# Kernel optimization log

Measured on AMD Instinct MI355X. Metric: run time of the kernel, lower is better.

## Reference

```python
import jax, jax.numpy as jnp
import numpy as np

B, C, H, W = 32, 512, 32, 32


def setup_inputs() -> dict:
    key = jax.random.key(0)
    ks = jax.random.split(key, 7)
    c2 = C // 2
    s_in = (1.0 / C) ** 0.5   # torch Conv2d default init scale (kernel 1x1)
    s_c2 = (1.0 / c2) ** 0.5
    return {
        "x": jax.random.normal(ks[0], (B, C, H, W), jnp.float32),
        "Wk": jax.random.normal(ks[1], (c2, C), jnp.float32) * s_in,
        "bk": jax.random.normal(ks[2], (c2,), jnp.float32) * s_in,
        "Wv": jax.random.normal(ks[3], (c2, C), jnp.float32) * s_in,
        "bv": jax.random.normal(ks[4], (c2,), jnp.float32) * s_in,
        "Wo": jax.random.normal(ks[5], (C, c2), jnp.float32) * s_c2,
        "bo": jax.random.normal(ks[6], (C,), jnp.float32) * s_c2,
    }


def reference(x, Wk, bk, Wv, bv, Wo, bo):
    Bn, Cn, Hn, Wn = x.shape
    c2 = Cn // 2
    M = Hn * Wn
    # 1x1 convs as channel contractions
    k = jnp.einsum('oc,bchw->bohw', Wk, x) + bk[None, :, None, None]   # [B,c2,H,W]
    v = jnp.einsum('oc,bchw->bohw', Wv, x) + bv[None, :, None, None]   # [B,c2,H,W]
    # torch .reshape(B, M, c2) reinterprets memory (NOT a transpose) -> same in jnp
    v = v.reshape(Bn, M, c2)                                           # [B,M,c2]
    kf = k.reshape(Bn, c2, M)                                          # [B,c2,M]
    # cov_feature: k^T I_hat k with I_hat = (1/M)I - (1/M^2)11^T
    #            = (1/M) k^T k - (1/M^2) s s^T,  s = sum over channels
    gram = jnp.einsum('bcm,bcn->bmn', kf, kf) / M                      # [B,M,M]
    s = kf.sum(axis=1)                                                 # [B,M]
    cov = gram - (s[:, :, None] * s[:, None, :]) / (M * M)
    attn = jax.nn.softmax(cov * (c2 ** -0.5), axis=-1)                 # [B,M,M]
    out = jnp.einsum('bmn,bnc->bmc', attn, v)                          # [B,M,c2]
    # torch .view(B, c2, H, W) is also a raw memory reinterpretation
    out = out.reshape(Bn, c2, Hn, Wn)
    out = jnp.einsum('oc,bchw->bohw', Wo, out) + bo[None, :, None, None]
    return out + x
```

## Files before the change

kernel.cpp:

```cpp
#include <hip/hip_runtime.h>


typedef short bf8 __attribute__((ext_vector_type(8)));
typedef float f32x4 __attribute__((ext_vector_type(4)));

#define MFMA16(a, b, c) __builtin_amdgcn_mfma_f32_16x16x32_bf16((a), (b), (c), 0, 0, 0)

__device__ __forceinline__ short f2bf(float x) {
  unsigned u = __float_as_uint(x);
  u += 0x7fffu + ((u >> 16) & 1u);
  return (short)(u >> 16);
}

__device__ __forceinline__ void gll16(const short* g, void* l) {
  __builtin_amdgcn_global_load_lds(
      (const __attribute__((address_space(1))) unsigned int*)g,
      (__attribute__((address_space(3))) unsigned int*)l, 16, 0, 0);
}

__device__ __forceinline__ void lgkm0() {
  asm volatile("s_waitcnt lgkmcnt(0)" ::: "memory");
}
template <int N>
__device__ __forceinline__ void waitv() {
  static_assert(N == 0 || N == 4 || N == 8, "bad vmcnt");
  if constexpr (N == 0) asm volatile("s_waitcnt vmcnt(0)" ::: "memory");
  else if constexpr (N == 4) asm volatile("s_waitcnt vmcnt(4)" ::: "memory");
  else asm volatile("s_waitcnt vmcnt(8)" ::: "memory");
}
__device__ __forceinline__ void barrier_relaxed() {
  asm volatile("" ::: "memory");
  __builtin_amdgcn_s_barrier();
  asm volatile("" ::: "memory");
}

__device__ __forceinline__ void gemm_core(const short* __restrict__ A,
                                          const short* __restrict__ B,
                                          int ldA, int ldB, int ksteps,
                                          char* smem, f32x4 acc[4][4]) {
  const int tid = threadIdx.x;
  const int w = tid >> 6, l = tid & 63;
  const int q = l >> 4, i = l & 15;
  const int wm = w & 1, wn = w >> 1;
  const int srow = l >> 3;
  const int gcol = ((l & 7) ^ srow) * 8;
  f32x4 zz = {0.f, 0.f, 0.f, 0.f};
  #pragma unroll
  for (int mt = 0; mt < 4; ++mt)
    #pragma unroll
    for (int nt = 0; nt < 4; ++nt) acc[mt][nt] = zz;

  for (int ks = 0; ks < ksteps; ++ks) {
    __syncthreads();
    const short* Ak = A + ks * 64 + gcol;
    const short* Bk = B + ks * 64 + gcol;
    #pragma unroll
    for (int j = 0; j < 4; ++j) {
      int s = w * 4 + j;
      size_t row = (size_t)(s * 8 + srow);
      gll16(Ak + row * ldA, smem + s * 1024);
      gll16(Bk + row * ldB, smem + 16384 + s * 1024);
    }
    __syncthreads();
    #pragma unroll
    for (int kq = 0; kq < 2; ++kq) {
      int sw = ((kq * 4 + q) ^ (i & 7)) * 16;
      bf8 af[4], bq[4];
      #pragma unroll
      for (int mt = 0; mt < 4; ++mt)
        af[mt] = *(const bf8*)(smem + (wm * 64 + mt * 16 + i) * 128 + sw);
      #pragma unroll
      for (int nt = 0; nt < 4; ++nt)
        bq[nt] = *(const bf8*)(smem + 16384 + (wn * 64 + nt * 16 + i) * 128 + sw);
      #pragma unroll
      for (int mt = 0; mt < 4; ++mt)
        #pragma unroll
        for (int nt = 0; nt < 4; ++nt)
          acc[mt][nt] = MFMA16(af[mt], bq[nt], acc[mt][nt]);
    }
  }
}

__global__ __launch_bounds__(256) void p0_xpose(const float* __restrict__ x,
                                                short* __restrict__ xT) {
  __shared__ float lds[64][65];
  int cb = blockIdx.x, sb = blockIdx.y, b = blockIdx.z;
  int t = threadIdx.x;
  int c0 = cb * 64, sp0 = sb * 64;
  const float4* x4 = reinterpret_cast<const float4*>(x);
  #pragma unroll
  for (int j = 0; j < 4; ++j) {
    int lin = t + 256 * j;
    int cl = lin >> 4, s4 = lin & 15;
    float4 v = x4[(((size_t)b * 512 + c0 + cl) * 1024 + sp0 + s4 * 4) >> 2];
    lds[cl][s4 * 4 + 0] = v.x; lds[cl][s4 * 4 + 1] = v.y;
    lds[cl][s4 * 4 + 2] = v.z; lds[cl][s4 * 4 + 3] = v.w;
  }
  __syncthreads();
  int spl = t >> 2, cs = (t & 3) * 16;
  bf8 o0, o1;
  #pragma unroll
  for (int j = 0; j < 8; ++j) o0[j] = f2bf(lds[cs + j][spl]);
  #pragma unroll
  for (int j = 0; j < 8; ++j) o1[j] = f2bf(lds[cs + 8 + j][spl]);
  size_t base = ((size_t)b * 1024 + sp0 + spl) * 512 + c0 + cs;
  *reinterpret_cast<bf8*>(xT + base) = o0;
  *reinterpret_cast<bf8*>(xT + base + 8) = o1;
}

__global__ __launch_bounds__(256) void w0_weights(const float* __restrict__ Wk,
                                                  const float* __restrict__ Wv,
                                                  const float* __restrict__ Wo,
                                                  short* __restrict__ Wkv_bf,
                                                  short* __restrict__ Wo_bf) {
  int g = blockIdx.x * 256 + threadIdx.x;
  if (g < 262144) {
    int o = g >> 9, c = g & 511;
    float v = (o < 256) ? Wk[o * 512 + c] : Wv[(o - 256) * 512 + c];
    Wkv_bf[g] = f2bf(v);
  } else {
    int i2 = g - 262144;
    Wo_bf[i2] = f2bf(Wo[i2]);
  }
}

__global__ __launch_bounds__(256, 2) void k1_kv(const short* __restrict__ xT,
                                                const short* __restrict__ Wkv,
                                                const float* __restrict__ bk,
                                                const float* __restrict__ bv,
                                                short* __restrict__ kT,
                                                short* __restrict__ vT,
                                                float* __restrict__ s_part) {
  __shared__ __attribute__((aligned(16))) char smem[36864];
  f32x4 acc[4][4];
  int bm = blockIdx.x, bn = blockIdx.y;
  gemm_core(xT + (size_t)bm * 128 * 512, Wkv + (size_t)bn * 128 * 512,
            512, 512, 8, smem, acc);
  int tid = threadIdx.x;
  int w = tid >> 6, l = tid & 63, q = l >> 4, i = l & 15;
  int wm = w & 1, wn = w >> 1;
  int mbase = bm * 128 + wm * 64;
  int nbase = bn * 128 + wn * 64;
  if (bn < 2) {
    __syncthreads();
    short* st = (short*)smem + w * 4352;
    float rp[4][4];
    #pragma unroll
    for (int mt = 0; mt < 4; ++mt)
      #pragma unroll
      for (int r = 0; r < 4; ++r) rp[mt][r] = 0.f;
    #pragma unroll
    for (int mt = 0; mt < 4; ++mt)
      #pragma unroll
      for (int nt = 0; nt < 4; ++nt) {
        float bias = bk[nbase + nt * 16 + i];
        #pragma unroll
        for (int r = 0; r < 4; ++r) {
          float val = acc[mt][nt][r] + bias;
          st[(mt * 16 + q * 4 + r) * 68 + nt * 16 + i] = f2bf(val);
          rp[mt][r] += val;
        }
      }
    lgkm0();
    #pragma unroll
    for (int j = 0; j < 8; ++j) {
      int row = j * 8 + (l >> 3), cc = l & 7;
      bf8 vv = *(const bf8*)(st + row * 68 + cc * 8);
      *(bf8*)(kT + (size_t)(mbase + row) * 256 + nbase + cc * 8) = vv;
    }
    #pragma unroll
    for (int mask = 1; mask <= 8; mask <<= 1)
      #pragma unroll
      for (int mt = 0; mt < 4; ++mt)
        #pragma unroll
        for (int r = 0; r < 4; ++r) rp[mt][r] += __shfl_xor(rp[mt][r], mask, 64);
    if (i == 0) {
      int pg = bn * 2 + wn;
      #pragma unroll
      for (int mt = 0; mt < 4; ++mt)
        #pragma unroll
        for (int r = 0; r < 4; ++r)
          s_part[pg * 32768 + mbase + mt * 16 + q * 4 + r] = rp[mt][r];
    }
  } else {
    #pragma unroll
    for (int mt = 0; mt < 4; ++mt)
      #pragma unroll
      for (int nt = 0; nt < 4; ++nt) {
        int o2 = nbase + nt * 16 + i - 256;
        float bias = bv[o2];
        #pragma unroll
        for (int r = 0; r < 4; ++r) {
          float val = acc[mt][nt][r] + bias;
          int mg = mbase + mt * 16 + q * 4 + r;
          int b = mg >> 10, sp = mg & 1023;
          vT[((size_t)b * 256 + (sp & 255)) * 1024 + 4 * o2 + (sp >> 8)] = f2bf(val);
        }
      }
  }
}

__global__ __launch_bounds__(256, 2) void k2_fused(const short* __restrict__ kT,
                                                   const short* __restrict__ vT,
                                                   const float* __restrict__ s_part,
                                                   short* __restrict__ OB) {
  __shared__ __attribute__((aligned(16))) char smem[81920];
  char* Apan = smem;
  char* Ppan = smem + 32768;
  char* Bst  = smem + 49152;

  const int id = blockIdx.x;
  const int xcd = id & 7, slot = id >> 3;
  const int b  = xcd * 4 + (slot >> 4);
  const int bm = slot & 15;

  const int tid = threadIdx.x;
  const int w = tid >> 6, l = tid & 63;
  const int q = l >> 4, i = l & 15;
  const int srow = l >> 3;
  const int gcol = ((l & 7) ^ srow) * 8;

  const short* kTb = kT + (size_t)b * 1024 * 256;
  const short* vTb = vT + (size_t)b * 256 * 1024;

  char* slabA = Bst + w * 4096;
  char* slabB = Bst + 16384 + w * 4096;

  const float sc1 = 1.0f / 16384.0f;
  const float sc2 = 1.0f / 16777216.0f;

  {
    const short* Am = kTb + (size_t)bm * 64 * 256;
    #pragma unroll
    for (int ks = 0; ks < 4; ++ks)
      #pragma unroll
      for (int j2 = 0; j2 < 2; ++j2) {
        int s2 = w * 2 + j2;
        gll16(Am + (size_t)(s2 * 8 + srow) * 256 + ks * 64 + gcol,
              Apan + ks * 8192 + s2 * 1024);
      }
  }

  const int mglob = b * 1024;
  float sm2[4][4];
  #pragma unroll
  for (int mt = 0; mt < 4; ++mt)
    #pragma unroll
    for (int r = 0; r < 4; ++r) {
      int m = mglob + bm * 64 + mt * 16 + q * 4 + r;
      sm2[mt][r] = (s_part[m] + s_part[32768 + m] + s_part[65536 + m] +
                    s_part[98304 + m]) * sc2;
    }
  float sn[8][2];
  #pragma unroll
  for (int c = 0; c < 8; ++c)
    #pragma unroll
    for (int nt = 0; nt < 2; ++nt) {
      int m = mglob + c * 128 + w * 32 + nt * 16 + i;
      sn[c][nt] = s_part[m] + s_part[32768 + m] + s_part[65536 + m] +
                  s_part[98304 + m];
    }

  auto stageS = [&](int c, int ks, char* sl) {
    const short* Bn = kTb + (size_t)c * 128 * 256 + ks * 64 + gcol;
    #pragma unroll
    for (int j = 0; j < 4; ++j)
      gll16(Bn + (size_t)(w * 32 + j * 8 + srow) * 256, sl + j * 1024);
  };
  auto stageV = [&](int c, int ks2, int h, char* sl) {
    const short* Vn = vTb + c * 128 + ks2 * 64 + gcol;
    #pragma unroll
    for (int j = 0; j < 4; ++j)
      gll16(Vn + (size_t)(w * 64 + h * 32 + j * 8 + srow) * 1024, sl + j * 1024);
  };

  stageS(0, 0, slabA);
  stageS(0, 1, slabB);
  waitv<8>();
  barrier_relaxed();

  f32x4 zz = {0.f, 0.f, 0.f, 0.f};
  f32x4 acc_o[4][4];
  float rowsum[4][4];
  #pragma unroll
  for (int mt = 0; mt < 4; ++mt)
    #pragma unroll
    for (int ct = 0; ct < 4; ++ct) acc_o[mt][ct] = zz;
  #pragma unroll
  for (int mt = 0; mt < 4; ++mt)
    #pragma unroll
    for (int r = 0; r < 4; ++r) rowsum[mt][r] = 0.f;

  #pragma unroll
  for (int c = 0; c < 8; ++c) {
    f32x4 acc_s[4][2];
    #pragma unroll
    for (int mt = 0; mt < 4; ++mt)
      #pragma unroll
      for (int nt = 0; nt < 2; ++nt) acc_s[mt][nt] = zz;

    #pragma unroll
    for (int ks = 0; ks < 4; ++ks) {
      char* sl = (ks & 1) ? slabB : slabA;
      waitv<4>();
      #pragma unroll
      for (int kq = 0; kq < 2; ++kq) {
        int sw = ((kq * 4 + q) ^ (i & 7)) * 16;
        bf8 af[4], bq2[2];
        #pragma unroll
        for (int mt = 0; mt < 4; ++mt)
          af[mt] = *(const bf8*)(Apan + ks * 8192 + (mt * 16 + i) * 128 + sw);
        #pragma unroll
        for (int nt = 0; nt < 2; ++nt)
          bq2[nt] = *(const bf8*)(sl + (nt * 16 + i) * 128 + sw);
        __builtin_amdgcn_s_setprio(1);
        #pragma unroll
        for (int mt = 0; mt < 4; ++mt)
          #pragma unroll
          for (int nt = 0; nt < 2; ++nt)
            acc_s[mt][nt] = MFMA16(af[mt], bq2[nt], acc_s[mt][nt]);
        __builtin_amdgcn_s_setprio(0);
      }
      lgkm0();
      if (ks < 2) stageS(c, ks + 2, sl);
      else        stageV(c, 0, ks - 2, sl);
    }

    barrier_relaxed();
    #pragma unroll
    for (int nt = 0; nt < 2; ++nt) {
      float snv = sn[c][nt];
      int nl = w * 32 + nt * 16 + i;
      char* pbase = Ppan + (nl >> 6) * 8192 + (nl & 7) * 2;
      int gchunk = (nl >> 3) & 7;
      #pragma unroll
      for (int mt = 0; mt < 4; ++mt)
        #pragma unroll
        for (int r = 0; r < 4; ++r) {
          int ml = mt * 16 + q * 4 + r;
          float p = __expf(acc_s[mt][nt][r] * sc1 - sm2[mt][r] * snv);
          rowsum[mt][r] += p;
          *(short*)(pbase + ml * 128 + ((gchunk ^ (ml & 7)) * 16)) = f2bf(p);
        }
    }
    lgkm0();
    barrier_relaxed();

    #pragma unroll
    for (int pv = 0; pv < 4; ++pv) {
      char* sl = (pv & 1) ? slabB : slabA;
      const int ks2 = pv >> 1, h = pv & 1;
      if (c == 7 && pv == 3) waitv<0>(); else waitv<4>();
      #pragma unroll
      for (int kq = 0; kq < 2; ++kq) {
        int sw = ((kq * 4 + q) ^ (i & 7)) * 16;
        bf8 ap[4], bv2[2];
        #pragma unroll
        for (int mt = 0; mt < 4; ++mt)
          ap[mt] = *(const bf8*)(Ppan + ks2 * 8192 + (mt * 16 + i) * 128 + sw);
        #pragma unroll
        for (int u = 0; u < 2; ++u)
          bv2[u] = *(const bf8*)(sl + (u * 16 + i) * 128 + sw);
        __builtin_amdgcn_s_setprio(1);
        #pragma unroll
        for (int mt = 0; mt < 4; ++mt)
          #pragma unroll
          for (int u = 0; u < 2; ++u)
            acc_o[mt][h * 2 + u] = MFMA16(ap[mt], bv2[u], acc_o[mt][h * 2 + u]);
        __builtin_amdgcn_s_setprio(0);
      }
      lgkm0();
      if (pv < 2) stageV(c, 1, pv, sl);
      else if (c < 7) stageS(c + 1, pv - 2, sl);
    }
  }

  #pragma unroll
  for (int mask = 1; mask <= 8; mask <<= 1)
    #pragma unroll
    for (int mt = 0; mt < 4; ++mt)
      #pragma unroll
      for (int r = 0; r < 4; ++r) rowsum[mt][r] += __shfl_xor(rowsum[mt][r], mask, 64);
  __syncthreads();
  float* rs = (float*)Ppan;
  if (i == 0) {
    #pragma unroll
    for (int mt = 0; mt < 4; ++mt)
      #pragma unroll
      for (int r = 0; r < 4; ++r)
        rs[w * 64 + mt * 16 + q * 4 + r] = rowsum[mt][r];
  }
  __syncthreads();
  float rinv[4][4];
  #pragma unroll
  for (int mt = 0; mt < 4; ++mt)
    #pragma unroll
    for (int r = 0; r < 4; ++r) {
      int m = mt * 16 + q * 4 + r;
      rinv[mt][r] = 1.0f / (rs[m] + rs[64 + m] + rs[128 + m] + rs[192 + m]);
    }
  short* ob = (short*)(Bst + w * 8192);
  #pragma unroll
  for (int mt = 0; mt < 4; ++mt)
    #pragma unroll
    for (int ct = 0; ct < 4; ++ct)
      #pragma unroll
      for (int r = 0; r < 4; ++r)
        ob[(r * 64 + ct * 16 + i) * 16 + mt * 4 + q] =
            f2bf(acc_o[mt][ct][r] * rinv[mt][r]);
  short* obg = OB + (size_t)b * 1024 * 256;
  #pragma unroll
  for (int jj = 0; jj < 8; ++jj) {
    int lr = jj * 32 + (l >> 1), ch = l & 1;
    bf8 vv = *(const bf8*)(ob + lr * 16 + ch * 8);
    int rr = lr >> 6, cc = lr & 63;
    *(bf8*)(obg + ((size_t)(rr * 256 + w * 64 + cc)) * 256 + bm * 16 + ch * 8) = vv;
  }
}

__global__ __launch_bounds__(256, 2) void k3_out(const short* __restrict__ Wo_bf,
                                                 const short* __restrict__ OB,
                                                 const float* __restrict__ bo,
                                                 const float* __restrict__ x,
                                                 float* __restrict__ out) {
  __shared__ __attribute__((aligned(16))) char smem[36864];
  f32x4 acc[4][4];
  int bm = blockIdx.x, bn = blockIdx.y, b = blockIdx.z;
  gemm_core(Wo_bf + (size_t)bm * 128 * 256,
            OB + ((size_t)b * 1024 + bn * 128) * 256, 256, 256, 4, smem, acc);
  int tid = threadIdx.x;
  int w = tid >> 6, l = tid & 63, q = l >> 4, i = l & 15;
  int wm = w & 1, wn = w >> 1;
  int oloc = bm * 128 + wm * 64, sploc = bn * 128 + wn * 64;
  __syncthreads();
  float* st = (float*)smem + w * 2112;
  #pragma unroll
  for (int half = 0; half < 2; ++half) {
    if (half) lgkm0();
    #pragma unroll
    for (int mtl = 0; mtl < 2; ++mtl) {
      int mt = half * 2 + mtl;
      #pragma unroll
      for (int nt = 0; nt < 4; ++nt)
        #pragma unroll
        for (int r = 0; r < 4; ++r)
          st[(mtl * 16 + q * 4 + r) * 66 + nt * 16 + i] = acc[mt][nt][r];
    }
    lgkm0();
    #pragma unroll
    for (int j = 0; j < 8; ++j) {
      int row = j * 4 + (l >> 4), c4 = l & 15;
      f32x4 v = *(const f32x4*)(st + row * 66 + c4 * 4);
      int o = oloc + half * 32 + row;
      int sp = sploc + c4 * 4;
      size_t idx = ((size_t)b * 512 + o) * 1024 + sp;
      float4 xv = *(const float4*)(x + idx);
      float bias = bo[o];
      float4 ov;
      ov.x = v[0] + bias + xv.x;
      ov.y = v[1] + bias + xv.y;
      ov.z = v[2] + bias + xv.z;
      ov.w = v[3] + bias + xv.w;
      *(float4*)(out + idx) = ov;
    }
  }
}

extern "C" void kernel_launch(void* const* d_in, const int* in_sizes, int n_in,
                              void* d_out, int out_size, void* d_ws, size_t ws_size,
                              hipStream_t stream) {
  (void)in_sizes; (void)n_in; (void)out_size; (void)ws_size;
  const float* x  = (const float*)d_in[0];
  const float* Wk = (const float*)d_in[1];
  const float* bk = (const float*)d_in[2];
  const float* Wv = (const float*)d_in[3];
  const float* bv = (const float*)d_in[4];
  const float* Wo = (const float*)d_in[5];
  const float* bo = (const float*)d_in[6];
  float* out = (float*)d_out;
  char* ws = (char*)d_ws;

  short* xT     = (short*)(ws);
  short* OB     = (short*)(ws);
  short* kTb    = (short*)(ws + 33554432);
  short* vTb    = (short*)(ws + 50331648);
  short* Wkv_bf = (short*)(ws + 67108864);
  short* Wo_bf  = (short*)(ws + 67633152);
  float* s_part = (float*)(ws + 67895296);

  p0_xpose<<<dim3(8, 16, 32), 256, 0, stream>>>(x, xT);
  w0_weights<<<1536, 256, 0, stream>>>(Wk, Wv, Wo, Wkv_bf, Wo_bf);
  k1_kv<<<dim3(256, 4), 256, 0, stream>>>(xT, Wkv_bf, bk, bv, kTb, vTb, s_part);
  k2_fused<<<dim3(512), 256, 0, stream>>>(kTb, vTb, s_part, OB);
  k3_out<<<dim3(4, 8, 32), 256, 0, stream>>>(Wo_bf, OB, bo, x, out);
}
```

Before: 237.0 us.

## Fuse transpose and weight-cast kernels; remap GEMM blocks for XCD-local L2 reuse

Merges the input transpose and the weight bf16 conversion into one launch, removing a kernel launch and its gap. Remaps the block indices of the k1 and k3 GEMMs so that blocks landing on the same XCD (round-robin by id&7) share A tiles or batch data. The aim is better L2 hit rates on the MI355X chiplet layout. The mapping assumes the hardware's round-robin dispatch of blocks across XCDs.

Result: faster. 222.5 us (-6.1%).

```diff
diff --git a/kernel.cpp b/kernel.cpp
--- a/kernel.cpp
+++ b/kernel.cpp
@@ -81,11 +81,29 @@
   }
 }
 
-__global__ __launch_bounds__(256) void p0_xpose(const float* __restrict__ x,
-                                                short* __restrict__ xT) {
+__global__ __launch_bounds__(256) void p0_fused(const float* __restrict__ x,
+                                                short* __restrict__ xT,
+                                                const float* __restrict__ Wk,
+                                                const float* __restrict__ Wv,
+                                                const float* __restrict__ Wo,
+                                                short* __restrict__ Wkv_bf,
+                                                short* __restrict__ Wo_bf) {
   __shared__ float lds[64][65];
-  int cb = blockIdx.x, sb = blockIdx.y, b = blockIdx.z;
+  int id = blockIdx.x;
   int t = threadIdx.x;
+  if (id >= 4096) {
+    int g = (id - 4096) * 256 + t;
+    if (g < 262144) {
+      int o = g >> 9, c = g & 511;
+      float v = (o < 256) ? Wk[o * 512 + c] : Wv[(o - 256) * 512 + c];
+      Wkv_bf[g] = f2bf(v);
+    } else {
+      int i2 = g - 262144;
+      Wo_bf[i2] = f2bf(Wo[i2]);
+    }
+    return;
+  }
+  int cb = id & 7, sb = (id >> 3) & 15, b = id >> 7;
   int c0 = cb * 64, sp0 = sb * 64;
   const float4* x4 = reinterpret_cast<const float4*>(x);
   #pragma unroll
@@ -106,22 +124,6 @@
   size_t base = ((size_t)b * 1024 + sp0 + spl) * 512 + c0 + cs;
   *reinterpret_cast<bf8*>(xT + base) = o0;
   *reinterpret_cast<bf8*>(xT + base + 8) = o1;
-}
-
-__global__ __launch_bounds__(256) void w0_weights(const float* __restrict__ Wk,
-                                                  const float* __restrict__ Wv,
-                                                  const float* __restrict__ Wo,
-                                                  short* __restrict__ Wkv_bf,
-                                                  short* __restrict__ Wo_bf) {
-  int g = blockIdx.x * 256 + threadIdx.x;
-  if (g < 262144) {
-    int o = g >> 9, c = g & 511;
-    float v = (o < 256) ? Wk[o * 512 + c] : Wv[(o - 256) * 512 + c];
-    Wkv_bf[g] = f2bf(v);
-  } else {
-    int i2 = g - 262144;
-    Wo_bf[i2] = f2bf(Wo[i2]);
-  }
 }
 
 __global__ __launch_bounds__(256, 2) void k1_kv(const short* __restrict__ xT,
@@ -133,7 +135,10 @@
                                                 float* __restrict__ s_part) {
   __shared__ __attribute__((aligned(16))) char smem[36864];
   f32x4 acc[4][4];
-  int bm = blockIdx.x, bn = blockIdx.y;
+  int id = blockIdx.x;
+  int xcd = id & 7, slot = id >> 3;
+  int bm = xcd * 32 + (slot >> 2);
+  int bn = slot & 3;
   gemm_core(xT + (size_t)bm * 128 * 512, Wkv + (size_t)bn * 128 * 512,
             512, 512, 8, smem, acc);
   int tid = threadIdx.x;
@@ -425,7 +430,11 @@
                                                  float* __restrict__ out) {
   __shared__ __attribute__((aligned(16))) char smem[36864];
   f32x4 acc[4][4];
-  int bm = blockIdx.x, bn = blockIdx.y, b = blockIdx.z;
+  int id = blockIdx.x;
+  int xcd = id & 7, slot = id >> 3;
+  int b = xcd * 4 + (slot >> 5);
+  int rem = slot & 31;
+  int bn = rem >> 2, bm = rem & 3;
   gemm_core(Wo_bf + (size_t)bm * 128 * 256,
             OB + ((size_t)b * 1024 + bn * 128) * 256, 256, 256, 4, smem, acc);
   int tid = threadIdx.x;
@@ -488,9 +497,8 @@
   short* Wo_bf  = (short*)(ws + 67633152);
   float* s_part = (float*)(ws + 67895296);
 
-  p0_xpose<<<dim3(8, 16, 32), 256, 0, stream>>>(x, xT);
-  w0_weights<<<1536, 256, 0, stream>>>(Wk, Wv, Wo, Wkv_bf, Wo_bf);
-  k1_kv<<<dim3(256, 4), 256, 0, stream>>>(xT, Wkv_bf, bk, bv, kTb, vTb, s_part);
-  k2_fused<<<dim3(512), 256, 0, stream>>>(kTb, vTb, s_part, OB);
-  k3_out<<<dim3(4, 8, 32), 256, 0, stream>>>(Wo_bf, OB, bo, x, out);
-}
+  p0_fused<<<5632, 256, 0, stream>>>(x, xT, Wk, Wv, Wo, Wkv_bf, Wo_bf);
+  k1_kv<<<1024, 256, 0, stream>>>(xT, Wkv_bf, bk, bv, kTb, vTb, s_part);
+  k2_fused<<<512, 256, 0, stream>>>(kTb, vTb, s_part, OB);
+  k3_out<<<1024, 256, 0, stream>>>(Wo_bf, OB, bo, x, out);
+}
```
